# Optimization experiments

Measured on AMD Instinct MI355X. Metric: run time of the kernel, lower is better.

## Reference

```python
import jax, jax.numpy as jnp
import numpy as np

E = 2048      # embed_size
H = 16        # heads_size
D_HEAD = E // H          # 128
D_ROPE = 32
SPLIT = D_HEAD - D_ROPE  # 96
C = 512       # d_kv_comp
B, S = 2, 2048
ROT_SCALE = 40.0


def _rotary_emb(seq_len):
    # inv_freq has d_rope//4 entries; emb is [S, d_rope//2]
    half = D_ROPE // 2
    inv_freq = 1.0 / (10000.0 ** (jnp.arange(0, half, 2, dtype=jnp.float32) / half))
    t = jnp.arange(seq_len, dtype=jnp.float32) / ROT_SCALE
    freqs = jnp.einsum('i,j->ij', t, inv_freq)
    return jnp.concatenate([freqs, freqs], axis=-1)  # [S, d_rope//2]


def _rotate_half(x):
    x1, x2 = jnp.split(x, 2, axis=-1)
    return jnp.concatenate([-x2, x1], axis=-1)


def _apply_rotary(x, cos, sin):
    rd = cos.shape[-1]
    x_rot, x_base = x[..., :rd], x[..., rd:]
    x_rot = x_rot * cos + _rotate_half(x_rot) * sin
    return jnp.concatenate([x_rot, x_base], axis=-1)


def setup_inputs() -> dict:
    key = jax.random.key(0)
    ks = jax.random.split(key, 10)

    def xav(k, shape):
        fan_in, fan_out = shape
        lim = float(np.sqrt(6.0 / (fan_in + fan_out)))
        return jax.random.uniform(k, shape, jnp.float32, -lim, lim)

    return {
        'h': jax.random.normal(ks[0], (B, S, E), jnp.float32),
        'W_dkv': xav(ks[1], (E, C)), 'b_dkv': jnp.zeros((C,), jnp.float32),
        'W_dq':  xav(ks[2], (E, C)), 'b_dq':  jnp.zeros((C,), jnp.float32),
        'W_uk':  xav(ks[3], (C, H * SPLIT)),  'b_uk': jnp.zeros((H * SPLIT,), jnp.float32),
        'W_uv':  xav(ks[4], (C, H * D_HEAD)), 'b_uv': jnp.zeros((H * D_HEAD,), jnp.float32),
        'W_uq':  xav(ks[5], (C, H * SPLIT)),  'b_uq': jnp.zeros((H * SPLIT,), jnp.float32),
        'W_qr':  xav(ks[6], (C, H * D_ROPE)), 'b_qr': jnp.zeros((H * D_ROPE,), jnp.float32),
        'W_kr':  xav(ks[7], (E, H * D_ROPE)), 'b_kr': jnp.zeros((H * D_ROPE,), jnp.float32),
        'W_out': xav(ks[8], (H * D_HEAD, E)), 'b_out': jnp.zeros((E,), jnp.float32),
    }


def reference(h, W_dkv, b_dkv, W_dq, b_dq, W_uk, b_uk, W_uv, b_uv,
              W_uq, b_uq, W_qr, b_qr, W_kr, b_kr, W_out, b_out):
    Bq, Sq, _ = h.shape
    c_kv = h @ W_dkv + b_dkv                                   # [B,S,C]
    k = (c_kv @ W_uk + b_uk).reshape(Bq, Sq, H, SPLIT)
    v = (c_kv @ W_uv + b_uv).reshape(Bq, Sq, H, D_HEAD)
    c_q = h @ W_dq + b_dq
    q_base = (c_q @ W_uq + b_uq).reshape(Bq, Sq, H, SPLIT)
    q_rot = (c_q @ W_qr + b_qr).reshape(Bq, Sq, H, D_ROPE)

    emb = _rotary_emb(Sq)                                      # [S, d_rope//2]
    cos = jnp.cos(emb)[None, :, None, :]
    sin = jnp.sin(emb)[None, :, None, :]
    q_rot = _apply_rotary(q_rot, cos, sin)
    k_rot = _apply_rotary((h @ W_kr + b_kr).reshape(Bq, Sq, H, D_ROPE), cos, sin)

    q = jnp.concatenate([q_base, q_rot], axis=-1)              # [B,S,H,d_head]
    k_full = jnp.concatenate([k, k_rot], axis=-1)

    scores = jnp.einsum('bqhd,bkhd->bhqk', q, k_full) / jnp.sqrt(jnp.float32(D_HEAD))
    causal = jnp.tril(jnp.ones((Sq, Sq), dtype=bool))
    scores = jnp.where(causal[None, None], scores, -jnp.inf)
    attn = jax.nn.softmax(scores, axis=-1)
    out = jnp.einsum('bhqk,bkhd->bqhd', attn, v).reshape(Bq, Sq, H * D_HEAD)
    out = out @ W_out + b_out
    return out, c_kv, k_rot
```

## Files before the change

kernel.cpp:

```cpp
#include <hip/hip_runtime.h>
#include <hip/hip_bf16.h>

#define B_   2
#define S_   2048
#define E_   2048
#define H_   16
#define DH_  128
#define DR_  32
#define SP_  96
#define C_   512
#define M_   (B_ * S_)

#define LOG2E 1.4426950408889634f

typedef __attribute__((ext_vector_type(8))) short short8;
typedef __attribute__((ext_vector_type(4))) float floatx4;

__device__ __forceinline__ float bfu(unsigned short u) {
  return __uint_as_float((unsigned)u << 16);
}
__device__ __forceinline__ unsigned short f2bf(float f) {
  unsigned u = __float_as_uint(f);
  return (unsigned short)((u + 0x7fff + ((u >> 16) & 1)) >> 16);
}

__device__ __forceinline__ void gload16(const void* g, void* l) {
  __builtin_amdgcn_global_load_lds(
      (const __attribute__((address_space(1))) void*)g,
      (__attribute__((address_space(3))) void*)l, 16, 0, 0);
}

__global__ __launch_bounds__(256) void f2bf_kernel(
    const float* __restrict__ src, unsigned short* __restrict__ dst) {
  size_t i = ((size_t)blockIdx.x * 256 + threadIdx.x) * 4;
  float4 v = *(const float4*)(src + i);
  ushort4 w;
  w.x = f2bf(v.x); w.y = f2bf(v.y); w.z = f2bf(v.z); w.w = f2bf(v.w);
  *(ushort4*)(dst + i) = w;
}

struct TEnt { const float* W; unsigned short* Wt; int K, N, ntiles, nx; };
struct TTab { TEnt e[8]; };

__global__ __launch_bounds__(256) void transpose_all_kernel(TTab tab) {
  __shared__ unsigned short T[32][33];
  int rem = blockIdx.x;
  const float* W = nullptr; unsigned short* Wt = nullptr;
  int K = 0, N = 0, nx = 1;
  bool done = false;
#pragma unroll
  for (int j = 0; j < 8; j++) {
    if (!done) {
      if (rem < tab.e[j].ntiles) {
        W = tab.e[j].W; Wt = tab.e[j].Wt;
        K = tab.e[j].K; N = tab.e[j].N; nx = tab.e[j].nx;
        done = true;
      } else {
        rem -= tab.e[j].ntiles;
      }
    }
  }
  int n0 = (rem % nx) * 32, k0 = (rem / nx) * 32;
  int t = threadIdx.x, lane = t & 31, grp = t >> 5;
#pragma unroll
  for (int p = 0; p < 4; p++) {
    int k = p * 8 + grp;
    T[lane][k] = f2bf(W[(size_t)(k0 + k) * N + n0 + lane]);
  }
  __syncthreads();
#pragma unroll
  for (int p = 0; p < 4; p++) {
    int n = p * 8 + grp;
    Wt[(size_t)(n0 + n) * K + k0 + lane] = T[n][lane];
  }
}

struct Seg {
  float* outF;
  unsigned short* outB;
  const float* bias;
  const float* biasM;
  int orow, chunk, gstride, obase, nstart, ileave;
  float oscale;
};

__global__ __launch_bounds__(256) void mfma_gemm(
    const unsigned short* __restrict__ A, const unsigned short* __restrict__ Wt,
    Seg s0, Seg s1, Seg s2, int K) {
  __shared__ unsigned short As0[128 * 32];
  __shared__ unsigned short Bs0[128 * 32];
  __shared__ unsigned short As1[128 * 32];
  __shared__ unsigned short Bs1[128 * 32];
  int tid = threadIdx.x;
  int lane = tid & 63, wave = tid >> 6;
  int l16 = lane & 15, quad = lane >> 4;

  int gx = gridDim.x;
  int nwg = gx * gridDim.y;
  int flat = blockIdx.y * gx + blockIdx.x;
  int w = (flat & 7) * (nwg >> 3) + (flat >> 3);
  int by = w / gx, bx = w - by * gx;
  int bm = by * 128, bn = bx * 128;
  int wm = (wave & 1) * 64, wn = (wave >> 1) * 64;

  floatx4 acc[4][4];
#pragma unroll
  for (int mt = 0; mt < 4; mt++)
#pragma unroll
    for (int nt = 0; nt < 4; nt++) acc[mt][nt] = (floatx4){0.f, 0.f, 0.f, 0.f};

  int c0 = wave * 2, c1 = c0 + 1;
  int srow = lane >> 2, scol = (lane & 3) * 8;
  const unsigned short* Ag0 = A + (size_t)(bm + c0 * 16 + srow) * K + scol;
  const unsigned short* Ag1 = A + (size_t)(bm + c1 * 16 + srow) * K + scol;
  const unsigned short* Bg0 = Wt + (size_t)(bn + c0 * 16 + srow) * K + scol;
  const unsigned short* Bg1 = Wt + (size_t)(bn + c1 * 16 + srow) * K + scol;

#define GSTAGE(kk, Asb, Bsb) do {            \
    gload16(Ag0 + (kk), &Asb[c0 * 512]);     \
    gload16(Ag1 + (kk), &Asb[c1 * 512]);     \
    gload16(Bg0 + (kk), &Bsb[c0 * 512]);     \
    gload16(Bg1 + (kk), &Bsb[c1 * 512]); } while (0)

#define GCOMPUTE(Asb, Bsb) do {                                            \
    short8 af[4], bfv[4];                                                  \
    _Pragma("unroll")                                                      \
    for (int mt = 0; mt < 4; mt++)                                         \
      af[mt] = *(const short8*)&Asb[(wm + mt * 16 + l16) * 32 + quad * 8]; \
    _Pragma("unroll")                                                      \
    for (int nt = 0; nt < 4; nt++)                                         \
      bfv[nt] = *(const short8*)&Bsb[(wn + nt * 16 + l16) * 32 + quad * 8];\
    _Pragma("unroll")                                                      \
    for (int mt = 0; mt < 4; mt++)                                         \
      _Pragma("unroll")                                                    \
      for (int nt = 0; nt < 4; nt++)                                       \
        acc[mt][nt] = __builtin_amdgcn_mfma_f32_16x16x32_bf16(             \
            af[mt], bfv[nt], acc[mt][nt], 0, 0, 0); } while (0)

  GSTAGE(0, As0, Bs0);
  __syncthreads();
  for (int k0 = 0; k0 < K; k0 += 64) {
    GSTAGE(k0 + 32, As1, Bs1);
    GCOMPUTE(As0, Bs0);
    __syncthreads();
    if (k0 + 64 < K) GSTAGE(k0 + 64, As0, Bs0);
    GCOMPUTE(As1, Bs1);
    __syncthreads();
  }
#undef GSTAGE
#undef GCOMPUTE

  Seg sg = (bn >= s2.nstart) ? s2 : ((bn >= s1.nstart) ? s1 : s0);

#pragma unroll
  for (int mt = 0; mt < 4; mt++) {
    int m0 = bm + wm + mt * 16 + quad * 4;
    float bm4[4] = {0.f, 0.f, 0.f, 0.f};
    if (sg.biasM) {
#pragma unroll
      for (int r = 0; r < 4; r++) bm4[r] = sg.biasM[m0 + r];
    }
#pragma unroll
    for (int nt = 0; nt < 4; nt++) {
      int n = bn + wn + nt * 16 + l16;
      int nl = n - sg.nstart;
      float bv = sg.biasM ? 0.f : sg.bias[nl];
      int ncol = sg.obase + (nl / sg.chunk) * sg.gstride + (nl % sg.chunk);
      if (sg.ileave)
        ncol = (ncol & ~31) | ((ncol & 15) << 1) | ((ncol >> 4) & 1);
#pragma unroll
      for (int r = 0; r < 4; r++) {
        float val = (acc[mt][nt][r] + (sg.biasM ? bm4[r] : bv)) * sg.oscale;
        size_t idx = (size_t)(m0 + r) * sg.orow + ncol;
        if (sg.outF) sg.outF[idx] = val;
        if (sg.outB) sg.outB[idx] = f2bf(val);
      }
    }
  }
}

__global__ __launch_bounds__(256) void rope_kernel(
    unsigned short* __restrict__ qf, unsigned short* __restrict__ kf,
    float* __restrict__ krot_out) {
  int idx = blockIdx.x * 256 + threadIdx.x;
  int j  = idx & 7;
  int h  = (idx >> 3) & (H_ - 1);
  int bs = idx >> 7;
  if (bs >= M_) return;
  int s = bs & (S_ - 1);
  float t = (float)s / 40.0f;
  float ang = t * exp2f(-1.6609640474436813f * (float)j);
  float c = cosf(ang), sn = sinf(ang);

  size_t base = (size_t)bs * 2048 + h * 128 + 96;
  float x0 = bfu(qf[base + j]), x1 = bfu(qf[base + j + 8]);
  qf[base + j]     = f2bf(x0 * c - x1 * sn);
  qf[base + j + 8] = f2bf(x1 * c + x0 * sn);

  float y0 = bfu(kf[base + j]), y1 = bfu(kf[base + j + 8]);
  float r0 = y0 * c - y1 * sn;
  float r1 = y1 * c + y0 * sn;
  kf[base + j]     = f2bf(r0);
  kf[base + j + 8] = f2bf(r1);

  size_t ko = (size_t)bs * (H_ * DR_) + h * DR_;
  krot_out[ko + j]      = r0;
  krot_out[ko + j + 8]  = r1;
  krot_out[ko + 16 + j] = bfu(kf[base + 16 + j]);
  krot_out[ko + 24 + j] = bfu(kf[base + 24 + j]);
}

#define PST 72
__global__ __launch_bounds__(256, 2) void attn_kernel(
    const unsigned short* __restrict__ qf, const unsigned short* __restrict__ kf,
    const unsigned short* __restrict__ vt, unsigned short* __restrict__ ao) {
  __shared__ unsigned short Ks[2][64 * 128];
  __shared__ unsigned short Vs[2][128 * 64];
  __shared__ unsigned short Ps[4][16 * PST];

  int bid0 = blockIdx.x;
  int xcd  = bid0 & 7;
  int idx  = bid0 >> 3;
  int bh   = xcd * 4 + (idx >> 4);
  int jp   = idx & 15;
  int h    = bh & 15;
  int b    = bh >> 4;
  int jjh  = 31 - jp;
  int jjl  = jp;
  int q0h  = jjh << 6, q0l = jjl << 6;
  int nchunks = jjh + 1;

  int tid  = threadIdx.x;
  int wave = tid >> 6;
  int lane = tid & 63;
  int l16  = lane & 15;
  int quad = lane >> 4;
  int x7   = l16 & 7;

  int krow = tid >> 2;
  int kst  = (tid & 3) * 4;
  int vrow = tid >> 1;
  int vst  = (tid & 1) * 4;
  const unsigned short* kg =
      kf + ((size_t)(b * S_ + krow)) * 2048 + h * 128 + kst * 8;
  const unsigned short* vg =
      vt + ((size_t)(h * 128 + vrow)) * 4096 + b * 2048 + vst * 8;
  int kwl[4], vwl[4];
#pragma unroll
  for (int i = 0; i < 4; i++) {
    kwl[i] = krow * 128 + (((kst + i) ^ (krow & 7)) * 8);
    vwl[i] = vrow * 64  + (((vst + i) ^ (vrow & 7)) * 8);
  }

  short8 qfh[4], qfl[4];
  {
    const unsigned short* qb =
        qf + ((size_t)(b * S_ + q0h + wave * 16 + l16)) * 2048 + h * 128 + quad * 8;
#pragma unroll
    for (int c = 0; c < 4; c++) qfh[c] = *(const short8*)(qb + c * 32);
  }
  {
    const unsigned short* qb =
        qf + ((size_t)(b * S_ + q0l + wave * 16 + l16)) * 2048 + h * 128 + quad * 8;
#pragma unroll
    for (int c = 0; c < 4; c++) qfl[c] = *(const short8*)(qb + c * 32);
  }

  floatx4 OaccH[8], OaccL[8];
#pragma unroll
  for (int dt = 0; dt < 8; dt++) {
    OaccH[dt] = (floatx4){0.f, 0.f, 0.f, 0.f};
    OaccL[dt] = (floatx4){0.f, 0.f, 0.f, 0.f};
  }
  float lpH[4] = {0.f, 0.f, 0.f, 0.f};
  float lpL[4] = {0.f, 0.f, 0.f, 0.f};
  int qgh = q0h + wave * 16;
  int qgl = q0l + wave * 16;

#define SCOMPUTE(QF, OC, LP, QG, DIAG) do {                                   \
    const unsigned short* Kc = Ks[cur];                                       \
    const unsigned short* Vc = Vs[cur];                                       \
    floatx4 sv[4];                                                            \
    _Pragma("unroll")                                                         \
    for (int nt = 0; nt < 4; nt++) sv[nt] = (floatx4){0.f, 0.f, 0.f, 0.f};    \
    __builtin_amdgcn_s_setprio(1);                                            \
    _Pragma("unroll")                                                         \
    for (int nt = 0; nt < 4; nt++)                                            \
      _Pragma("unroll")                                                       \
      for (int c = 0; c < 4; c++) {                                           \
        short8 kfr = *(const short8*)&Kc[(nt * 16 + l16) * 128 +              \
                                         ((4 * c + quad) ^ x7) * 8];          \
        sv[nt] = __builtin_amdgcn_mfma_f32_16x16x32_bf16(QF[c], kfr, sv[nt],  \
                                                         0, 0, 0);            \
      }                                                                       \
    __builtin_amdgcn_s_setprio(0);                                            \
    unsigned short* P = Ps[wave];                                             \
    _Pragma("unroll")                                                         \
    for (int ks = 0; ks < 2; ks++)                                            \
      _Pragma("unroll")                                                       \
      for (int r = 0; r < 4; r++) {                                           \
        float p0 = exp2f(fminf(sv[2 * ks][r], 80.f));                         \
        float p1 = exp2f(fminf(sv[2 * ks + 1][r], 80.f));                     \
        if (DIAG) {                                                           \
          int q_r = QG + quad * 4 + r;                                        \
          int kc0 = kt0 + ks * 32 + l16;                                      \
          if (kc0 > q_r)      p0 = 0.f;                                       \
          if (kc0 + 16 > q_r) p1 = 0.f;                                       \
        }                                                                     \
        unsigned pk;                                                          \
        asm("v_cvt_pk_bf16_f32 %0, %1, %2" : "=v"(pk) : "v"(p0), "v"(p1));    \
        *(unsigned*)&P[(quad * 4 + r) * PST + ks * 32 + 2 * l16] = pk;        \
        LP[r] += p0 + p1;                                                     \
      }                                                                       \
    short8 pf0 = *(const short8*)&P[l16 * PST + quad * 8];                    \
    short8 pf1 = *(const short8*)&P[l16 * PST + 32 + quad * 8];               \
    __builtin_amdgcn_s_setprio(1);                                            \
    _Pragma("unroll")                                                         \
    for (int dt = 0; dt < 8; dt++) {                                          \
      short8 vf0 = *(const short8*)&Vc[(dt * 16 + l16) * 64 +                 \
                                       ((quad) ^ x7) * 8];                    \
      OC[dt] = __builtin_amdgcn_mfma_f32_16x16x32_bf16(pf0, vf0, OC[dt],      \
                                                       0, 0, 0);              \
      short8 vf1 = *(const short8*)&Vc[(dt * 16 + l16) * 64 +                 \
                                       ((4 + quad) ^ x7) * 8];                \
      OC[dt] = __builtin_amdgcn_mfma_f32_16x16x32_bf16(pf1, vf1, OC[dt],      \
                                                       0, 0, 0);              \
    }                                                                         \
    __builtin_amdgcn_s_setprio(0);                                            \
  } while (0)

  short8 kr[4], vr[4];
#pragma unroll
  for (int i = 0; i < 4; i++) {
    kr[i] = *(const short8*)(kg + i * 8);
    vr[i] = *(const short8*)(vg + i * 8);
  }
#pragma unroll
  for (int i = 0; i < 4; i++) {
    *(short8*)&Ks[0][kwl[i]] = kr[i];
    *(short8*)&Vs[0][vwl[i]] = vr[i];
  }
#pragma unroll
  for (int i = 0; i < 4; i++) {
    kr[i] = *(const short8*)(kg + 131072 + i * 8);
    vr[i] = *(const short8*)(vg + 64 + i * 8);
  }
  __syncthreads();

  int cur = 0;
  for (int t = 0; t < nchunks; t++) {
#pragma unroll
    for (int i = 0; i < 4; i++) {
      *(short8*)&Ks[cur ^ 1][kwl[i]] = kr[i];
      *(short8*)&Vs[cur ^ 1][vwl[i]] = vr[i];
    }
    {
      int tf = (t + 2 < nchunks) ? t + 2 : nchunks - 1;
      const unsigned short* ksrc = kg + (size_t)tf * 131072;
      const unsigned short* vsrc = vg + tf * 64;
#pragma unroll
      for (int i = 0; i < 4; i++) {
        kr[i] = *(const short8*)(ksrc + i * 8);
        vr[i] = *(const short8*)(vsrc + i * 8);
      }
    }
    int kt0 = t << 6;
    SCOMPUTE(qfh, OaccH, lpH, qgh, (t == jjh));
    if (t <= jjl) SCOMPUTE(qfl, OaccL, lpL, qgl, (t == jjl));
    __syncthreads();
    cur ^= 1;
  }
#undef SCOMPUTE

#pragma unroll
  for (int side = 0; side < 2; side++) {
    floatx4* OC = side ? OaccL : OaccH;
    float*   LP = side ? lpL : lpH;
    int qg = (side ? qgl : qgh) + quad * 4;
    float linv[4];
#pragma unroll
    for (int r = 0; r < 4; r++) {
      float ls = LP[r];
#pragma unroll
      for (int sh = 1; sh < 16; sh <<= 1) ls += __shfl_xor(ls, sh);
      linv[r] = 1.0f / ls;
    }
#pragma unroll
    for (int r = 0; r < 4; r++) {
      unsigned short* dst =
          ao + ((size_t)(b * S_ + qg + r)) * 2048 + h * 128 + l16;
#pragma unroll
      for (int dt = 0; dt < 8; dt++) dst[dt * 16] = f2bf(OC[dt][r] * linv[r]);
    }
  }
}

static inline Seg mkseg(float* oF, unsigned short* oB, const float* bias,
                        const float* biasM, int orow, int chunk, int gstride,
                        int obase, int nstart, int ileave, float oscale) {
  Seg s;
  s.outF = oF; s.outB = oB; s.bias = bias; s.biasM = biasM;
  s.orow = orow; s.chunk = chunk; s.gstride = gstride;
  s.obase = obase; s.nstart = nstart; s.ileave = ileave; s.oscale = oscale;
  return s;
}
static inline Seg segnone() {
  return mkseg(nullptr, nullptr, nullptr, nullptr, 1, 1, 1, 0, 0x7fffffff, 0, 1.f);
}
static inline TEnt mktent(const float* W, unsigned short* Wt, int K, int N,
                          int ntiles, int nx) {
  TEnt e;
  e.W = W; e.Wt = Wt; e.K = K; e.N = N; e.ntiles = ntiles; e.nx = nx;
  return e;
}

extern "C" void kernel_launch(void* const* d_in, const int* in_sizes, int n_in,
                              void* d_out, int out_size, void* d_ws, size_t ws_size,
                              hipStream_t stream) {
  const float* h     = (const float*)d_in[0];
  const float* W_dkv = (const float*)d_in[1];
  const float* b_dkv = (const float*)d_in[2];
  const float* W_dq  = (const float*)d_in[3];
  const float* b_dq  = (const float*)d_in[4];
  const float* W_uk  = (const float*)d_in[5];
  const float* b_uk  = (const float*)d_in[6];
  const float* W_uv  = (const float*)d_in[7];
  const float* b_uv  = (const float*)d_in[8];
  const float* W_uq  = (const float*)d_in[9];
  const float* b_uq  = (const float*)d_in[10];
  const float* W_qr  = (const float*)d_in[11];
  const float* b_qr  = (const float*)d_in[12];
  const float* W_kr  = (const float*)d_in[13];
  const float* b_kr  = (const float*)d_in[14];
  const float* W_out = (const float*)d_in[15];
  const float* b_out = (const float*)d_in[16];

  float* out      = (float*)d_out;
  float* out_ckv  = out + (size_t)M_ * E_;
  float* out_krot = out_ckv + (size_t)M_ * C_;

  unsigned short* w16 = (unsigned short*)d_ws;
  unsigned short* h_bf   = w16;
  unsigned short* q_bf   = w16 + 8388608;
  unsigned short* k_bf   = w16 + 16777216;
  unsigned short* vt_bf  = w16 + 25165824;
  unsigned short* ao_bf  = w16 + 33554432;
  unsigned short* ckv_bf = w16 + 41943040;
  unsigned short* cq_bf  = w16 + 44040192;
  unsigned short* Wt_dkv = w16 + 46137344;
  unsigned short* Wt_dq  = w16 + 47185920;
  unsigned short* Wt_kr  = w16 + 48234496;
  unsigned short* Wt_uk  = w16 + 49283072;
  unsigned short* Wt_uv  = w16 + 50069504;
  unsigned short* Wt_uq  = w16 + 51118080;
  unsigned short* Wt_qr  = w16 + 51904512;
  unsigned short* Wt_out = w16 + 52166656;

  dim3 blk(256);
  const float qscale = 0.08838834764831845f * LOG2E;

  f2bf_kernel<<<8192, blk, 0, stream>>>(h, h_bf);

  TTab tab;
  tab.e[0] = mktent(W_dkv, Wt_dkv, E_, C_,       1024, 16);
  tab.e[1] = mktent(W_dq,  Wt_dq,  E_, C_,       1024, 16);
  tab.e[2] = mktent(W_kr,  Wt_kr,  E_, H_ * DR_, 1024, 16);
  tab.e[3] = mktent(W_uk,  Wt_uk,  C_, H_ * SP_,  768, 48);
  tab.e[4] = mktent(W_uv,  Wt_uv,  C_, H_ * DH_, 1024, 64);
  tab.e[5] = mktent(W_uq,  Wt_uq,  C_, H_ * SP_,  768, 48);
  tab.e[6] = mktent(W_qr,  Wt_qr,  C_, H_ * DR_,  256, 16);
  tab.e[7] = mktent(W_out, Wt_out, E_, E_,       4096, 64);
  transpose_all_kernel<<<9984, blk, 0, stream>>>(tab);

  mfma_gemm<<<dim3(1536 / 128, M_ / 128), blk, 0, stream>>>(
      h_bf, Wt_dkv,
      mkseg(out_ckv, ckv_bf, b_dkv, nullptr, C_, C_, C_, 0, 0, 0, 1.f),
      mkseg(nullptr, cq_bf,  b_dq,  nullptr, C_, C_, C_, 0, 512, 0, 1.f),
      mkseg(nullptr, k_bf,   b_kr,  nullptr, 2048, DR_, DH_, SP_, 1024, 0, 1.f),
      E_);
  mfma_gemm<<<dim3((H_ * SP_) / 128, M_ / 128), blk, 0, stream>>>(
      ckv_bf, Wt_uk,
      mkseg(nullptr, k_bf, b_uk, nullptr, 2048, SP_, DH_, 0, 0, 0, 1.f),
      segnone(), segnone(), C_);
  mfma_gemm<<<dim3(M_ / 128, (H_ * DH_) / 128), blk, 0, stream>>>(
      Wt_uv, ckv_bf,
      mkseg(nullptr, vt_bf, nullptr, b_uv, M_, M_, M_, 0, 0, 1, 1.f),
      segnone(), segnone(), C_);
  mfma_gemm<<<dim3(2048 / 128, M_ / 128), blk, 0, stream>>>(
      cq_bf, Wt_uq,
      mkseg(nullptr, q_bf, b_uq, nullptr, 2048, SP_, DH_, 0, 0, 0, qscale),
      mkseg(nullptr, q_bf, b_qr, nullptr, 2048, DR_, DH_, SP_, 1536, 0, qscale),
      segnone(), C_);

  rope_kernel<<<(M_ * H_ * 8) / 256, blk, 0, stream>>>(q_bf, k_bf, out_krot);
  attn_kernel<<<B_ * H_ * 16, blk, 0, stream>>>(q_bf, k_bf, vt_bf, ao_bf);

  mfma_gemm<<<dim3(E_ / 128, M_ / 128), blk, 0, stream>>>(
      ao_bf, Wt_out,
      mkseg(out, nullptr, b_out, nullptr, E_, E_, E_, 0, 0, 0, 1.f),
      segnone(), segnone(), E_);
}
```

Before: 368.5 us.

## Rewrite attention with 32x32 MFMA tiles, async LDS staging, per-wave query roles

The attention kernel moves from 16x16x32 to 32x32x16 bf16 MFMA. Each wave now owns a 32-row query slice, with waves split between the high and low causal tile pair instead of every wave processing both. K/V tiles are staged straight into LDS with global_load_lds, replacing the register round-trip, and the P buffer uses a swizzled layout. The rope interleave mapping in the GEMM epilogue changes to a 64-wide pattern to match the new Q/K fragment layout. This cuts LDS reads per FLOP and register staging, but waves on the low tile sit idle during most iterations, which may cause load imbalance.

```diff
diff --git a/kernel.cpp b/kernel.cpp
--- a/kernel.cpp
+++ b/kernel.cpp
@@ -15,6 +15,7 @@
 
 typedef __attribute__((ext_vector_type(8))) short short8;
 typedef __attribute__((ext_vector_type(4))) float floatx4;
+typedef __attribute__((ext_vector_type(16))) float floatx16;
 
 __device__ __forceinline__ float bfu(unsigned short u) {
   return __uint_as_float((unsigned)u << 16);
@@ -167,7 +168,7 @@
       float bv = sg.biasM ? 0.f : sg.bias[nl];
       int ncol = sg.obase + (nl / sg.chunk) * sg.gstride + (nl % sg.chunk);
       if (sg.ileave)
-        ncol = (ncol & ~31) | ((ncol & 15) << 1) | ((ncol >> 4) & 1);
+        ncol = (ncol & ~63) | ((ncol & 31) << 1) | ((ncol >> 5) & 1);
 #pragma unroll
       for (int r = 0; r < 4; r++) {
         float val = (acc[mt][nt][r] + (sg.biasM ? bm4[r] : bv)) * sg.oscale;
@@ -210,13 +211,12 @@
   krot_out[ko + 24 + j] = bfu(kf[base + 24 + j]);
 }
 
-#define PST 72
 __global__ __launch_bounds__(256, 2) void attn_kernel(
     const unsigned short* __restrict__ qf, const unsigned short* __restrict__ kf,
     const unsigned short* __restrict__ vt, unsigned short* __restrict__ ao) {
   __shared__ unsigned short Ks[2][64 * 128];
   __shared__ unsigned short Vs[2][128 * 64];
-  __shared__ unsigned short Ps[4][16 * PST];
+  __shared__ unsigned short Ps[4][32 * 64];
 
   int bid0 = blockIdx.x;
   int xcd  = bid0 & 7;
@@ -225,173 +225,137 @@
   int jp   = idx & 15;
   int h    = bh & 15;
   int b    = bh >> 4;
-  int jjh  = 31 - jp;
-  int jjl  = jp;
-  int q0h  = jjh << 6, q0l = jjl << 6;
-  int nchunks = jjh + 1;
+  int jjh  = 31 - jp, jjl = jp;
 
   int tid  = threadIdx.x;
   int wave = tid >> 6;
   int lane = tid & 63;
-  int l16  = lane & 15;
-  int quad = lane >> 4;
-  int x7   = l16 & 7;
-
-  int krow = tid >> 2;
-  int kst  = (tid & 3) * 4;
-  int vrow = tid >> 1;
-  int vst  = (tid & 1) * 4;
-  const unsigned short* kg =
-      kf + ((size_t)(b * S_ + krow)) * 2048 + h * 128 + kst * 8;
-  const unsigned short* vg =
-      vt + ((size_t)(h * 128 + vrow)) * 4096 + b * 2048 + vst * 8;
-  int kwl[4], vwl[4];
-#pragma unroll
-  for (int i = 0; i < 4; i++) {
-    kwl[i] = krow * 128 + (((kst + i) ^ (krow & 7)) * 8);
-    vwl[i] = vrow * 64  + (((vst + i) ^ (vrow & 7)) * 8);
-  }
-
-  short8 qfh[4], qfl[4];
+  int l32  = lane & 31;
+  int hl   = lane >> 5;
+  int x7   = l32 & 7;
+
+  int role = wave ^ ((bid0 & 1) << 1);
+  int jt   = (role < 2) ? jjh : jjl;
+  int qg   = ((role < 2) ? jjh : jjl) * 64 + (role & 1) * 32;
+
+  const unsigned short* kp0; const unsigned short* kp1;
+  const unsigned short* kp2; const unsigned short* kp3;
+  const unsigned short* vp0; const unsigned short* vp1;
+  const unsigned short* vp2; const unsigned short* vp3;
+  {
+    int l4 = lane >> 4, l3 = lane >> 3;
+#define KSRC(i) (kf + ((size_t)(b * S_ + 16 * wave + 4 * (i) + l4)) * 2048 + \
+                 h * 128 + (((lane & 15) ^ ((16 * wave + 4 * (i) + l4) & 7)) * 8))
+#define VSRC(i) (vt + ((size_t)(h * 128 + 32 * wave + 8 * (i) + l3)) * 4096 + \
+                 b * 2048 + (((lane & 7) ^ ((32 * wave + 8 * (i) + l3) & 7)) * 8))
+    kp0 = KSRC(0); kp1 = KSRC(1); kp2 = KSRC(2); kp3 = KSRC(3);
+    vp0 = VSRC(0); vp1 = VSRC(1); vp2 = VSRC(2); vp3 = VSRC(3);
+#undef KSRC
+#undef VSRC
+  }
+  int ldso = wave * 2048;
+
+#define STAGE(tt, bb) do {                                                   \
+    size_t ko_ = (size_t)(tt) * 131072; int vo_ = (tt) * 64;                 \
+    gload16(kp0 + ko_, &Ks[bb][ldso]);                                       \
+    gload16(kp1 + ko_, &Ks[bb][ldso + 512]);                                 \
+    gload16(kp2 + ko_, &Ks[bb][ldso + 1024]);                                \
+    gload16(kp3 + ko_, &Ks[bb][ldso + 1536]);                                \
+    gload16(vp0 + vo_, &Vs[bb][ldso]);                                       \
+    gload16(vp1 + vo_, &Vs[bb][ldso + 512]);                                 \
+    gload16(vp2 + vo_, &Vs[bb][ldso + 1024]);                                \
+    gload16(vp3 + vo_, &Vs[bb][ldso + 1536]); } while (0)
+
+  short8 qfr[8];
   {
     const unsigned short* qb =
-        qf + ((size_t)(b * S_ + q0h + wave * 16 + l16)) * 2048 + h * 128 + quad * 8;
-#pragma unroll
-    for (int c = 0; c < 4; c++) qfh[c] = *(const short8*)(qb + c * 32);
-  }
-  {
-    const unsigned short* qb =
-        qf + ((size_t)(b * S_ + q0l + wave * 16 + l16)) * 2048 + h * 128 + quad * 8;
-#pragma unroll
-    for (int c = 0; c < 4; c++) qfl[c] = *(const short8*)(qb + c * 32);
-  }
-
-  floatx4 OaccH[8], OaccL[8];
-#pragma unroll
-  for (int dt = 0; dt < 8; dt++) {
-    OaccH[dt] = (floatx4){0.f, 0.f, 0.f, 0.f};
-    OaccL[dt] = (floatx4){0.f, 0.f, 0.f, 0.f};
-  }
-  float lpH[4] = {0.f, 0.f, 0.f, 0.f};
-  float lpL[4] = {0.f, 0.f, 0.f, 0.f};
-  int qgh = q0h + wave * 16;
-  int qgl = q0l + wave * 16;
-
-#define SCOMPUTE(QF, OC, LP, QG, DIAG) do {                                   \
-    const unsigned short* Kc = Ks[cur];                                       \
-    const unsigned short* Vc = Vs[cur];                                       \
-    floatx4 sv[4];                                                            \
-    _Pragma("unroll")                                                         \
-    for (int nt = 0; nt < 4; nt++) sv[nt] = (floatx4){0.f, 0.f, 0.f, 0.f};    \
-    __builtin_amdgcn_s_setprio(1);                                            \
-    _Pragma("unroll")                                                         \
-    for (int nt = 0; nt < 4; nt++)                                            \
-      _Pragma("unroll")                                                       \
-      for (int c = 0; c < 4; c++) {                                           \
-        short8 kfr = *(const short8*)&Kc[(nt * 16 + l16) * 128 +              \
-                                         ((4 * c + quad) ^ x7) * 8];          \
-        sv[nt] = __builtin_amdgcn_mfma_f32_16x16x32_bf16(QF[c], kfr, sv[nt],  \
-                                                         0, 0, 0);            \
-      }                                                                       \
-    __builtin_amdgcn_s_setprio(0);                                            \
-    unsigned short* P = Ps[wave];                                             \
-    _Pragma("unroll")                                                         \
-    for (int ks = 0; ks < 2; ks++)                                            \
-      _Pragma("unroll")                                                       \
-      for (int r = 0; r < 4; r++) {                                           \
-        float p0 = exp2f(fminf(sv[2 * ks][r], 80.f));                         \
-        float p1 = exp2f(fminf(sv[2 * ks + 1][r], 80.f));                     \
-        if (DIAG) {                                                           \
-          int q_r = QG + quad * 4 + r;                                        \
-          int kc0 = kt0 + ks * 32 + l16;                                      \
-          if (kc0 > q_r)      p0 = 0.f;                                       \
-          if (kc0 + 16 > q_r) p1 = 0.f;                                       \
-        }                                                                     \
-        unsigned pk;                                                          \
-        asm("v_cvt_pk_bf16_f32 %0, %1, %2" : "=v"(pk) : "v"(p0), "v"(p1));    \
-        *(unsigned*)&P[(quad * 4 + r) * PST + ks * 32 + 2 * l16] = pk;        \
-        LP[r] += p0 + p1;                                                     \
-      }                                                                       \
-    short8 pf0 = *(const short8*)&P[l16 * PST + quad * 8];                    \
-    short8 pf1 = *(const short8*)&P[l16 * PST + 32 + quad * 8];               \
-    __builtin_amdgcn_s_setprio(1);                                            \
-    _Pragma("unroll")                                                         \
-    for (int dt = 0; dt < 8; dt++) {                                          \
-      short8 vf0 = *(const short8*)&Vc[(dt * 16 + l16) * 64 +                 \
-                                       ((quad) ^ x7) * 8];                    \
-      OC[dt] = __builtin_amdgcn_mfma_f32_16x16x32_bf16(pf0, vf0, OC[dt],      \
-                                                       0, 0, 0);              \
-      short8 vf1 = *(const short8*)&Vc[(dt * 16 + l16) * 64 +                 \
-                                       ((4 + quad) ^ x7) * 8];                \
-      OC[dt] = __builtin_amdgcn_mfma_f32_16x16x32_bf16(pf1, vf1, OC[dt],      \
-                                                       0, 0, 0);              \
-    }                                                                         \
-    __builtin_amdgcn_s_setprio(0);                                            \
-  } while (0)
-
-  short8 kr[4], vr[4];
-#pragma unroll
-  for (int i = 0; i < 4; i++) {
-    kr[i] = *(const short8*)(kg + i * 8);
-    vr[i] = *(const short8*)(vg + i * 8);
-  }
-#pragma unroll
-  for (int i = 0; i < 4; i++) {
-    *(short8*)&Ks[0][kwl[i]] = kr[i];
-    *(short8*)&Vs[0][vwl[i]] = vr[i];
-  }
-#pragma unroll
-  for (int i = 0; i < 4; i++) {
-    kr[i] = *(const short8*)(kg + 131072 + i * 8);
-    vr[i] = *(const short8*)(vg + 64 + i * 8);
-  }
+        qf + ((size_t)(b * S_ + qg + l32)) * 2048 + h * 128 + hl * 8;
+#pragma unroll
+    for (int c = 0; c < 8; c++) qfr[c] = *(const short8*)(qb + c * 16);
+  }
+
+  floatx16 Oa[4];
+  float lp[16];
+#pragma unroll
+  for (int dt = 0; dt < 4; dt++)
+#pragma unroll
+    for (int r = 0; r < 16; r++) Oa[dt][r] = 0.f;
+#pragma unroll
+  for (int r = 0; r < 16; r++) lp[r] = 0.f;
+
+  int nkt = jjh + 1;
+
+  STAGE(0, 0);
   __syncthreads();
 
   int cur = 0;
-  for (int t = 0; t < nchunks; t++) {
-#pragma unroll
-    for (int i = 0; i < 4; i++) {
-      *(short8*)&Ks[cur ^ 1][kwl[i]] = kr[i];
-      *(short8*)&Vs[cur ^ 1][vwl[i]] = vr[i];
+  for (int t = 0; t < nkt; t++) {
+    if (t + 1 < nkt) STAGE(t + 1, cur ^ 1);
+    if (t <= jt) {
+      const unsigned short* Kc = Ks[cur];
+      const unsigned short* Vc = Vs[cur];
+      floatx16 s0, s1;
+#pragma unroll
+      for (int r = 0; r < 16; r++) { s0[r] = 0.f; s1[r] = 0.f; }
+      __builtin_amdgcn_s_setprio(1);
+#pragma unroll
+      for (int c = 0; c < 8; c++) {
+        short8 k0 = *(const short8*)&Kc[l32 * 128 + (((c * 2 + hl) ^ x7)) * 8];
+        s0 = __builtin_amdgcn_mfma_f32_32x32x16_bf16(qfr[c], k0, s0, 0, 0, 0);
+        short8 k1 = *(const short8*)&Kc[(32 + l32) * 128 + (((c * 2 + hl) ^ x7)) * 8];
+        s1 = __builtin_amdgcn_mfma_f32_32x32x16_bf16(qfr[c], k1, s1, 0, 0, 0);
+      }
+      __builtin_amdgcn_s_setprio(0);
+      int kt0 = t << 6;
+      bool diag = (t == jt);
+      unsigned short* Pw = Ps[wave];
+#pragma unroll
+      for (int r = 0; r < 16; r++) {
+        float p0 = exp2f(fminf(s0[r], 80.f));
+        float p1 = exp2f(fminf(s1[r], 80.f));
+        int qrow = (r & 3) + 8 * (r >> 2) + 4 * hl;
+        if (diag) {
+          int q_r = qg + qrow;
+          if (kt0 + l32 > q_r)      p0 = 0.f;
+          if (kt0 + 32 + l32 > q_r) p1 = 0.f;
+        }
+        unsigned pk;
+        asm("v_cvt_pk_bf16_f32 %0, %1, %2" : "=v"(pk) : "v"(p0), "v"(p1));
+        *(unsigned*)&Pw[qrow * 64 + (((l32 >> 2) ^ ((r & 3) + 4 * hl)) * 8) +
+                        2 * (l32 & 3)] = pk;
+        lp[r] += p0 + p1;
+      }
+      __builtin_amdgcn_s_setprio(1);
+#pragma unroll
+      for (int kkc = 0; kkc < 4; kkc++) {
+        short8 pa = *(const short8*)&Pw[l32 * 64 + (((kkc * 2 + hl) ^ x7)) * 8];
+#pragma unroll
+        for (int dt = 0; dt < 4; dt++) {
+          short8 vf = *(const short8*)&Vc[(dt * 32 + l32) * 64 +
+                                          (((kkc * 2 + hl) ^ x7)) * 8];
+          Oa[dt] = __builtin_amdgcn_mfma_f32_32x32x16_bf16(pa, vf, Oa[dt], 0, 0, 0);
+        }
+      }
+      __builtin_amdgcn_s_setprio(0);
     }
-    {
-      int tf = (t + 2 < nchunks) ? t + 2 : nchunks - 1;
-      const unsigned short* ksrc = kg + (size_t)tf * 131072;
-      const unsigned short* vsrc = vg + tf * 64;
-#pragma unroll
-      for (int i = 0; i < 4; i++) {
-        kr[i] = *(const short8*)(ksrc + i * 8);
-        vr[i] = *(const short8*)(vsrc + i * 8);
-      }
-    }
-    int kt0 = t << 6;
-    SCOMPUTE(qfh, OaccH, lpH, qgh, (t == jjh));
-    if (t <= jjl) SCOMPUTE(qfl, OaccL, lpL, qgl, (t == jjl));
     __syncthreads();
     cur ^= 1;
   }
-#undef SCOMPUTE
-
-#pragma unroll
-  for (int side = 0; side < 2; side++) {
-    floatx4* OC = side ? OaccL : OaccH;
-    float*   LP = side ? lpL : lpH;
-    int qg = (side ? qgl : qgh) + quad * 4;
-    float linv[4];
-#pragma unroll
-    for (int r = 0; r < 4; r++) {
-      float ls = LP[r];
-#pragma unroll
-      for (int sh = 1; sh < 16; sh <<= 1) ls += __shfl_xor(ls, sh);
-      linv[r] = 1.0f / ls;
-    }
-#pragma unroll
-    for (int r = 0; r < 4; r++) {
-      unsigned short* dst =
-          ao + ((size_t)(b * S_ + qg + r)) * 2048 + h * 128 + l16;
-#pragma unroll
-      for (int dt = 0; dt < 8; dt++) dst[dt * 16] = f2bf(OC[dt][r] * linv[r]);
-    }
+#undef STAGE
+
+#pragma unroll
+  for (int r = 0; r < 16; r++) {
+    float ls = lp[r];
+#pragma unroll
+    for (int sh = 1; sh < 32; sh <<= 1) ls += __shfl_xor(ls, sh);
+    lp[r] = 1.0f / ls;
+  }
+#pragma unroll
+  for (int r = 0; r < 16; r++) {
+    int qrow = qg + (r & 3) + 8 * (r >> 2) + 4 * hl;
+    unsigned short* dst = ao + ((size_t)(b * S_ + qrow)) * 2048 + h * 128 + l32;
+#pragma unroll
+    for (int dt = 0; dt < 4; dt++) dst[dt * 32] = f2bf(Oa[dt][r] * lp[r]);
   }
 }
 
```

Result: slower. 396.2 us (+7.5%).

## Merge prep kernels and fuse three up-projection GEMMs into one launch

Applied to the files above, without the earlier changes.

Folds the h-to-bf16 conversion into the weight-transpose kernel, and merges the three small up-projection GEMMs (K, V-transposed, Q) into one 1408-block launch that dispatches on block index with an XCD-aware remap. It also changes the attention block-to-work mapping so heavy and light causal rows are interleaved differently across XCDs. The intent is to cut launch overhead and the tail idle time of the small GEMMs. The cost is per-block branching and a different L2 locality pattern.

```diff
diff --git a/kernel.cpp b/kernel.cpp
--- a/kernel.cpp
+++ b/kernel.cpp
@@ -30,21 +30,22 @@
       (__attribute__((address_space(3))) void*)l, 16, 0, 0);
 }
 
-__global__ __launch_bounds__(256) void f2bf_kernel(
-    const float* __restrict__ src, unsigned short* __restrict__ dst) {
-  size_t i = ((size_t)blockIdx.x * 256 + threadIdx.x) * 4;
-  float4 v = *(const float4*)(src + i);
-  ushort4 w;
-  w.x = f2bf(v.x); w.y = f2bf(v.y); w.z = f2bf(v.z); w.w = f2bf(v.w);
-  *(ushort4*)(dst + i) = w;
-}
-
 struct TEnt { const float* W; unsigned short* Wt; int K, N, ntiles, nx; };
 struct TTab { TEnt e[8]; };
 
-__global__ __launch_bounds__(256) void transpose_all_kernel(TTab tab) {
+__global__ __launch_bounds__(256) void prep_kernel(
+    const float* __restrict__ hsrc, unsigned short* __restrict__ hdst,
+    TTab tab) {
+  if (blockIdx.x < 8192) {
+    size_t i = ((size_t)blockIdx.x * 256 + threadIdx.x) * 4;
+    float4 v = *(const float4*)(hsrc + i);
+    ushort4 w;
+    w.x = f2bf(v.x); w.y = f2bf(v.y); w.z = f2bf(v.z); w.w = f2bf(v.w);
+    *(ushort4*)(hdst + i) = w;
+    return;
+  }
   __shared__ unsigned short T[32][33];
-  int rem = blockIdx.x;
+  int rem = blockIdx.x - 8192;
   const float* W = nullptr; unsigned short* Wt = nullptr;
   int K = 0, N = 0, nx = 1;
   bool done = false;
@@ -84,9 +85,9 @@
   float oscale;
 };
 
-__global__ __launch_bounds__(256) void mfma_gemm(
-    const unsigned short* __restrict__ A, const unsigned short* __restrict__ Wt,
-    Seg s0, Seg s1, Seg s2, int K) {
+__device__ __forceinline__ void gemm_body(
+    const unsigned short* __restrict__ A, const unsigned short* __restrict__ W,
+    int K, int bm, int bn, const Seg& sg) {
   __shared__ unsigned short As0[128 * 32];
   __shared__ unsigned short Bs0[128 * 32];
   __shared__ unsigned short As1[128 * 32];
@@ -94,13 +95,6 @@
   int tid = threadIdx.x;
   int lane = tid & 63, wave = tid >> 6;
   int l16 = lane & 15, quad = lane >> 4;
-
-  int gx = gridDim.x;
-  int nwg = gx * gridDim.y;
-  int flat = blockIdx.y * gx + blockIdx.x;
-  int w = (flat & 7) * (nwg >> 3) + (flat >> 3);
-  int by = w / gx, bx = w - by * gx;
-  int bm = by * 128, bn = bx * 128;
   int wm = (wave & 1) * 64, wn = (wave >> 1) * 64;
 
   floatx4 acc[4][4];
@@ -113,8 +107,8 @@
   int srow = lane >> 2, scol = (lane & 3) * 8;
   const unsigned short* Ag0 = A + (size_t)(bm + c0 * 16 + srow) * K + scol;
   const unsigned short* Ag1 = A + (size_t)(bm + c1 * 16 + srow) * K + scol;
-  const unsigned short* Bg0 = Wt + (size_t)(bn + c0 * 16 + srow) * K + scol;
-  const unsigned short* Bg1 = Wt + (size_t)(bn + c1 * 16 + srow) * K + scol;
+  const unsigned short* Bg0 = W + (size_t)(bn + c0 * 16 + srow) * K + scol;
+  const unsigned short* Bg1 = W + (size_t)(bn + c1 * 16 + srow) * K + scol;
 
 #define GSTAGE(kk, Asb, Bsb) do {            \
     gload16(Ag0 + (kk), &Asb[c0 * 512]);     \
@@ -150,8 +144,6 @@
 #undef GSTAGE
 #undef GCOMPUTE
 
-  Seg sg = (bn >= s2.nstart) ? s2 : ((bn >= s1.nstart) ? s1 : s0);
-
 #pragma unroll
   for (int mt = 0; mt < 4; mt++) {
     int m0 = bm + wm + mt * 16 + quad * 4;
@@ -177,6 +169,63 @@
       }
     }
   }
+}
+
+__global__ __launch_bounds__(256) void mfma_gemm(
+    const unsigned short* __restrict__ A, const unsigned short* __restrict__ Wt,
+    Seg s0, Seg s1, Seg s2, int K) {
+  int gx = gridDim.x;
+  int nwg = gx * gridDim.y;
+  int flat = blockIdx.y * gx + blockIdx.x;
+  int w = (flat & 7) * (nwg >> 3) + (flat >> 3);
+  int by = w / gx, bx = w - by * gx;
+  int bm = by * 128, bn = bx * 128;
+  Seg sg = (bn >= s2.nstart) ? s2 : ((bn >= s1.nstart) ? s1 : s0);
+  gemm_body(A, Wt, K, bm, bn, sg);
+}
+
+__global__ __launch_bounds__(256) void fused_gemm3(
+    const unsigned short* __restrict__ ckv, const unsigned short* __restrict__ cq,
+    const unsigned short* __restrict__ wuk, const unsigned short* __restrict__ wuv,
+    const unsigned short* __restrict__ wuq,
+    unsigned short* __restrict__ kbf, unsigned short* __restrict__ vtbf,
+    unsigned short* __restrict__ qbf,
+    const float* __restrict__ b_uk, const float* __restrict__ b_uv,
+    const float* __restrict__ b_uq, const float* __restrict__ b_qr,
+    float qscale) {
+  int flat = blockIdx.x;
+  int w = (flat & 7) * 176 + (flat >> 3);
+  const unsigned short* A; const unsigned short* W;
+  int bm, bn;
+  Seg sg;
+  sg.outF = nullptr; sg.oscale = 1.f; sg.ileave = 0; sg.nstart = 0;
+  if (w < 384) {
+    int by = w / 12, bx = w - by * 12;
+    bm = by * 128; bn = bx * 128;
+    A = ckv; W = wuk;
+    sg.outB = kbf; sg.bias = b_uk; sg.biasM = nullptr;
+    sg.orow = 2048; sg.chunk = SP_; sg.gstride = DH_; sg.obase = 0;
+  } else if (w < 896) {
+    int w2 = w - 384;
+    int by = w2 >> 5, bx = w2 & 31;
+    bm = by * 128; bn = bx * 128;
+    A = wuv; W = ckv;
+    sg.outB = vtbf; sg.bias = nullptr; sg.biasM = b_uv;
+    sg.orow = M_; sg.chunk = M_; sg.gstride = M_; sg.obase = 0; sg.ileave = 1;
+  } else {
+    int w3 = w - 896;
+    int by = w3 >> 4, bx = w3 & 15;
+    bm = by * 128; bn = bx * 128;
+    A = cq; W = wuq;
+    sg.outB = qbf; sg.biasM = nullptr; sg.orow = 2048; sg.oscale = qscale;
+    if (bn >= 1536) {
+      sg.bias = b_qr; sg.chunk = DR_; sg.gstride = DH_; sg.obase = SP_;
+      sg.nstart = 1536;
+    } else {
+      sg.bias = b_uq; sg.chunk = SP_; sg.gstride = DH_; sg.obase = 0;
+    }
+  }
+  gemm_body(A, W, 512, bm, bn, sg);
 }
 
 __global__ __launch_bounds__(256) void rope_kernel(
@@ -221,8 +270,10 @@
   int bid0 = blockIdx.x;
   int xcd  = bid0 & 7;
   int idx  = bid0 >> 3;
-  int bh   = xcd * 4 + (idx >> 4);
-  int jp   = idx & 15;
+  int r_   = idx >> 5;
+  int q_   = idx & 31;
+  int bh   = xcd * 4 + (q_ >> 3);
+  int jp   = r_ ? (15 - (q_ & 7)) : (q_ & 7);
   int h    = bh & 15;
   int b    = bh >> 4;
   int jjh  = 31 - jp;
@@ -455,11 +506,10 @@
   unsigned short* Wt_uq  = w16 + 51118080;
   unsigned short* Wt_qr  = w16 + 51904512;
   unsigned short* Wt_out = w16 + 52166656;
+  (void)Wt_qr;
 
   dim3 blk(256);
   const float qscale = 0.08838834764831845f * LOG2E;
-
-  f2bf_kernel<<<8192, blk, 0, stream>>>(h, h_bf);
 
   TTab tab;
   tab.e[0] = mktent(W_dkv, Wt_dkv, E_, C_,       1024, 16);
@@ -468,9 +518,9 @@
   tab.e[3] = mktent(W_uk,  Wt_uk,  C_, H_ * SP_,  768, 48);
   tab.e[4] = mktent(W_uv,  Wt_uv,  C_, H_ * DH_, 1024, 64);
   tab.e[5] = mktent(W_uq,  Wt_uq,  C_, H_ * SP_,  768, 48);
-  tab.e[6] = mktent(W_qr,  Wt_qr,  C_, H_ * DR_,  256, 16);
+  tab.e[6] = mktent(W_qr,  w16 + 51904512, C_, H_ * DR_,  256, 16);
   tab.e[7] = mktent(W_out, Wt_out, E_, E_,       4096, 64);
-  transpose_all_kernel<<<9984, blk, 0, stream>>>(tab);
+  prep_kernel<<<18176, blk, 0, stream>>>(h, h_bf, tab);
 
   mfma_gemm<<<dim3(1536 / 128, M_ / 128), blk, 0, stream>>>(
       h_bf, Wt_dkv,
@@ -478,19 +528,10 @@
       mkseg(nullptr, cq_bf,  b_dq,  nullptr, C_, C_, C_, 0, 512, 0, 1.f),
       mkseg(nullptr, k_bf,   b_kr,  nullptr, 2048, DR_, DH_, SP_, 1024, 0, 1.f),
       E_);
-  mfma_gemm<<<dim3((H_ * SP_) / 128, M_ / 128), blk, 0, stream>>>(
-      ckv_bf, Wt_uk,
-      mkseg(nullptr, k_bf, b_uk, nullptr, 2048, SP_, DH_, 0, 0, 0, 1.f),
-      segnone(), segnone(), C_);
-  mfma_gemm<<<dim3(M_ / 128, (H_ * DH_) / 128), blk, 0, stream>>>(
-      Wt_uv, ckv_bf,
-      mkseg(nullptr, vt_bf, nullptr, b_uv, M_, M_, M_, 0, 0, 1, 1.f),
-      segnone(), segnone(), C_);
-  mfma_gemm<<<dim3(2048 / 128, M_ / 128), blk, 0, stream>>>(
-      cq_bf, Wt_uq,
-      mkseg(nullptr, q_bf, b_uq, nullptr, 2048, SP_, DH_, 0, 0, 0, qscale),
-      mkseg(nullptr, q_bf, b_qr, nullptr, 2048, DR_, DH_, SP_, 1536, 0, qscale),
-      segnone(), C_);
+
+  fused_gemm3<<<1408, blk, 0, stream>>>(
+      ckv_bf, cq_bf, Wt_uk, Wt_uv, Wt_uq, k_bf, vt_bf, q_bf,
+      b_uk, b_uv, b_uq, b_qr, qscale);
 
   rope_kernel<<<(M_ * H_ * 8) / 256, blk, 0, stream>>>(q_bf, k_bf, out_krot);
   attn_kernel<<<B_ * H_ * 16, blk, 0, stream>>>(q_bf, k_bf, vt_bf, ao_bf);
```

New measurement: 353.7 us. 4.0% less time.
